# Optimization experiments

Hardware: AMD Instinct MI355X
Metric: run time of the kernel (lower is better)

Reference implementation:

```python
import jax, jax.numpy as jnp
import numpy as np

B, T, I, H, O = 64, 2000, 2, 512, 1
DT, TAU = 10.0, 100.0
EXCIT = 0.8
SIG_REC, SIG_IN = 0.01, 0.01
ALPHA = DT / TAU
IN_SCALE = float(np.sqrt(2.0 * (DT / TAU) * SIG_IN ** 2))
REC_SCALE = float(np.sqrt(2.0 * (TAU / DT) * SIG_REC ** 2))


def setup_inputs() -> dict:
    key = jax.random.key(0)
    ks = jax.random.split(key, 8)
    xav = lambda k, shp, gain: gain * np.sqrt(2.0 / (shp[0] + shp[1])) * jax.random.normal(k, shp, jnp.float32)
    return {
        "i_stim": jax.random.normal(ks[0], (B, T), jnp.float32),
        "i_cc": jax.random.normal(ks[1], (B, T), jnp.float32),
        "hidden": jnp.zeros((B, H), jnp.float32),
        "w_ih": xav(ks[2], (H, I), 1.0),
        "b_ih": jnp.zeros((H,), jnp.float32),
        "w_hh": jax.nn.relu(xav(ks[3], (H, H), 0.1)),  # init applies relu to w_hh
        "b_hh": jnp.zeros((H,), jnp.float32),
        "w_ho": xav(ks[4], (O, H), 1.0),
        "b_ho": jnp.zeros((O,), jnp.float32),
    }


def reference(i_stim, i_cc, hidden, w_ih, b_ih, w_hh, b_hh, w_ho, b_ho):
    ei = jnp.where(jnp.arange(H) < int(EXCIT * H), 1.0, -1.0).astype(w_hh.dtype)
    w_hh_ei = jnp.abs(w_hh * (1.0 - jnp.eye(H, dtype=w_hh.dtype))) * ei  # [H,H], time-invariant

    inputs = jnp.stack([i_stim, i_cc], axis=-1).transpose(1, 0, 2)  # [T,B,2]
    nk = jax.random.key(42)
    n_in = jax.random.normal(jax.random.fold_in(nk, 0), (T, B, I), inputs.dtype)
    n_rec = jax.random.normal(jax.random.fold_in(nk, 1), (T, B, H), hidden.dtype)

    def step(h, xs):
        x_t, ni, nr = xs
        cur = jax.nn.relu(x_t + IN_SCALE * ni)  # training=True path
        hid_in = cur @ w_ih.T  # [B,H]; note b_ih is never added (faithful to source)
        hid_hid = jax.nn.relu(h) @ w_hh_ei.T + b_hh + REC_SCALE * nr
        h_new = h + (-h + hid_in + hid_hid) * ALPHA
        out = jax.nn.relu(h_new) @ w_ho.T + b_ho  # [B,O]
        return h_new, (out, h_new)

    _, (outs, hids) = jax.lax.scan(step, hidden, (inputs, n_in, n_rec))
    return outs.transpose(1, 0, 2), hids.transpose(1, 0, 2)  # [B,T,O], [B,T,H]
```

## Files before the change

kernel.cpp:

```cpp
#include <hip/hip_runtime.h>
#include <stdint.h>
#include <math.h>

#define HH   512
#define BB   64
#define TT   2000
#define NEXC 409
#define SLICE  128
#define NBLK   (BB * 4)

constexpr float ALPHA_F     = 0.1f;
constexpr float IN_SCALE_F  = (float)4.4721359549995794e-03;
constexpr float REC_SCALE_F = (float)4.4721359549995794e-02;
constexpr float SQRT2_F     = 1.41421356237309515f;
constexpr float U_LO        = -0x1.fffffep-1f;

struct U2 { uint32_t a, b; };

__host__ __device__ constexpr uint32_t rotl32(uint32_t x, int d) {
  return (x << d) | (x >> (32 - d));
}

__host__ __device__ constexpr U2 tf2x32(uint32_t k0, uint32_t k1,
                                        uint32_t x0, uint32_t x1) {
  uint32_t ks[3] = {k0, k1, k0 ^ k1 ^ 0x1BD11BDAu};
  const int R[2][4] = {{13, 15, 26, 6}, {17, 29, 16, 24}};
  x0 += ks[0]; x1 += ks[1];
  for (int g = 0; g < 5; ++g) {
    const int* r = R[g & 1];
    for (int i = 0; i < 4; ++i) { x0 += x1; x1 = rotl32(x1, r[i]); x1 ^= x0; }
    x0 += ks[(g + 1) % 3];
    x1 += ks[(g + 2) % 3] + (uint32_t)(g + 1);
  }
  return U2{x0, x1};
}

constexpr U2 KIN_  = tf2x32(0u, 42u, 0u, 0u);
constexpr U2 KREC_ = tf2x32(0u, 42u, 0u, 1u);
constexpr uint32_t KIN0 = KIN_.a,  KIN1 = KIN_.b;
constexpr uint32_t KRC0 = KREC_.a, KRC1 = KREC_.b;

__device__ __forceinline__ float jax_normal(uint32_t k0, uint32_t k1, uint32_t idx) {
  U2 o = tf2x32(k0, k1, 0u, idx);
  uint32_t bits = o.a ^ o.b;
  float f = __uint_as_float((bits >> 9) | 0x3f800000u) - 1.0f;
  float u = fmaxf(U_LO, f * 2.0f + U_LO);
  float w = -log1pf(-u * u);
  float p;
  if (w < 5.0f) {
    w = w - 2.5f;
    p =             2.81022636e-08f;
    p = fmaf(p, w,  3.43273939e-07f);
    p = fmaf(p, w, -3.5233877e-06f);
    p = fmaf(p, w, -4.39150654e-06f);
    p = fmaf(p, w,  0.00021858087f);
    p = fmaf(p, w, -0.00125372503f);
    p = fmaf(p, w, -0.00417768164f);
    p = fmaf(p, w,  0.246640727f);
    p = fmaf(p, w,  1.50140941f);
  } else {
    w = sqrtf(w) - 3.0f;
    p =            -0.000200214257f;
    p = fmaf(p, w,  0.000100950558f);
    p = fmaf(p, w,  0.00134934322f);
    p = fmaf(p, w, -0.00367342844f);
    p = fmaf(p, w,  0.00573950773f);
    p = fmaf(p, w, -0.0076224613f);
    p = fmaf(p, w,  0.00943887047f);
    p = fmaf(p, w,  1.00167406f);
    p = fmaf(p, w,  2.83297682f);
  }
  return SQRT2_F * (p * u);
}

#define PUB_WORDS (2 * BB * HH)
#define PUB_BYTES (PUB_WORDS * 8)

__global__ __launch_bounds__(512, 2)
void zrnn_main(const float* __restrict__ i_stim, const float* __restrict__ i_cc,
               const float* __restrict__ hidden0,
               const float* __restrict__ w_ih, const float* __restrict__ w_hh,
               const float* __restrict__ b_hh,
               const float* __restrict__ w_ho, const float* __restrict__ b_ho,
               float* __restrict__ outs, float* __restrict__ hids,
               uint64_t* __restrict__ pub) {
  const int bid  = blockIdx.x;
  const int low3 = bid & 7;
  const int q    = bid >> 3;
  const int s    = q & 3;
  const int b    = ((q >> 2) << 3) + low3;
  const int tid  = threadIdx.x;
  const int lane = tid & 63;
  const int wv   = tid >> 6;

  const int  ownLo = s * SLICE;
  const bool isOwn = (tid >= ownLo) && (tid < ownLo + SLICE);
  const int  jloc  = tid - ownLo;

  __shared__ float stim_s[TT];
  __shared__ float cc_s[TT];
  __shared__ float red[2][8][SLICE];
  __shared__ float nbuf[4][SLICE];
  __shared__ float nin_s[4][2];
  __shared__ float obuf[8];

  for (int idx = tid; idx < TT; idx += 512) {
    stim_s[idx] = i_stim[b * TT + idx];
    cc_s[idx]   = i_cc[b * TT + idx];
  }

  const int jA = ownLo + lane;
  const int jB = jA + 64;
  const int i0 = wv * 64;
  float wA[64], wB[64];
  #pragma unroll
  for (int k4 = 0; k4 < 16; ++k4) {
    float4 a4 = *reinterpret_cast<const float4*>(&w_hh[jA * HH + i0 + k4 * 4]);
    float4 b4 = *reinterpret_cast<const float4*>(&w_hh[jB * HH + i0 + k4 * 4]);
    const float av[4] = {a4.x, a4.y, a4.z, a4.w};
    const float bv[4] = {b4.x, b4.y, b4.z, b4.w};
    #pragma unroll
    for (int c = 0; c < 4; ++c) {
      const int i = i0 + k4 * 4 + c;
      float va = (i == jA) ? 0.0f : fabsf(av[c]);
      float vb = (i == jB) ? 0.0f : fabsf(bv[c]);
      wA[k4 * 4 + c] = (i < NEXC) ? va : -va;
      wB[k4 * 4 + c] = (i < NEXC) ? vb : -vb;
    }
  }

  float h = 0.0f, wih0 = 0.0f, wih1 = 0.0f, bhh = 0.0f;
  if (isOwn) {
    h    = hidden0[b * HH + tid];
    wih0 = w_ih[tid * 2 + 0];
    wih1 = w_ih[tid * 2 + 1];
    bhh  = b_hh[tid];
  }
  const float who_f = w_ho[tid];
  const float bho   = b_ho[0];

  float rv = fmaxf(hidden0[b * HH + tid], 0.0f);

  if (isOwn) {
    #pragma unroll
    for (int tp = 0; tp < 4; ++tp)
      nbuf[tp][jloc] = jax_normal(KRC0, KRC1,
          (uint32_t)tp * (uint32_t)(BB * HH) + (uint32_t)(b * HH + tid));
    if (jloc < 8)
      nin_s[jloc >> 1][jloc & 1] = jax_normal(KIN0, KIN1,
          (uint32_t)((jloc >> 1) * (BB * 2) + b * 2 + (jloc & 1)));
  }

  uint64_t* pub_b0 = pub + (size_t)b * HH;
  uint64_t* pub_b1 = pub + (size_t)(BB + b) * HH;
  float* __restrict__ hid_out = hids + (size_t)b * TT * HH;

  __syncthreads();

  for (int t = 0; t < TT; ++t) {
    const int par = t & 1;

    if (t > 0 && s == ((t - 1) & 3)) {
      float v = rv * who_f;
      #pragma unroll
      for (int off = 32; off > 0; off >>= 1) v += __shfl_down(v, off);
      if (lane == 0) obuf[wv] = v;
    }

    float nr = 0.0f, ni0 = 0.0f, ni1 = 0.0f, x0 = 0.0f, x1 = 0.0f;
    if (isOwn) {
      nr  = nbuf[t & 3][jloc];
      ni0 = nin_s[t & 3][0];
      ni1 = nin_s[t & 3][1];
      x0  = stim_s[t];
      x1  = cc_s[t];
    }

    float accA = 0.0f, accB = 0.0f;
    #pragma unroll
    for (int k = 0; k < 64; ++k) {
      float rk = __uint_as_float(__builtin_amdgcn_readlane(__float_as_uint(rv), k));
      accA = fmaf(rk, wA[k], accA);
      accB = fmaf(rk, wB[k], accB);
    }
    red[par][wv][lane]      = accA;
    red[par][wv][64 + lane] = accB;
    __syncthreads();

    uint64_t* pub_t = par ? pub_b1 : pub_b0;

    if (isOwn) {
      float acc = red[par][0][jloc];
      #pragma unroll
      for (int w = 1; w < 8; ++w) acc += red[par][w][jloc];
      float hid_hid = acc + bhh + REC_SCALE_F * nr;
      float cur0 = fmaxf(x0 + IN_SCALE_F * ni0, 0.0f);
      float cur1 = fmaxf(x1 + IN_SCALE_F * ni1, 0.0f);
      float hid_in = cur0 * wih0 + cur1 * wih1;
      h = h + (-h + hid_in + hid_hid) * ALPHA_F;
      float r = fmaxf(h, 0.0f);
      uint64_t wd = ((uint64_t)(uint32_t)(t + 1) << 32) |
                    (uint64_t)__float_as_uint(r);
      __hip_atomic_store(&pub_t[tid], wd, __ATOMIC_RELAXED,
                         __HIP_MEMORY_SCOPE_AGENT);
      rv = r;
      __builtin_nontemporal_store(h, hid_out + (size_t)t * HH + tid);

      if (tid == ownLo && t > 0 && s == ((t - 1) & 3)) {
        float psum = ((obuf[0] + obuf[1]) + (obuf[2] + obuf[3])) +
                     ((obuf[4] + obuf[5]) + (obuf[6] + obuf[7]));
        outs[b * TT + (t - 1)] = psum + bho;
      }

      if (t + 4 < TT) {
        nbuf[t & 3][jloc] = jax_normal(KRC0, KRC1,
            (uint32_t)(t + 4) * (uint32_t)(BB * HH) + (uint32_t)(b * HH + tid));
        if (jloc < 2)
          nin_s[t & 3][jloc] = jax_normal(KIN0, KIN1,
              (uint32_t)((t + 4) * (BB * 2) + b * 2 + jloc));
      }
    } else {
      const uint32_t tagw = (uint32_t)(t + 1);
      uint64_t w = __hip_atomic_load(&pub_t[tid], __ATOMIC_RELAXED,
                                     __HIP_MEMORY_SCOPE_AGENT);
      if ((uint32_t)(w >> 32) != tagw) {
        uint64_t w2 = __hip_atomic_load(&pub_t[tid], __ATOMIC_RELAXED,
                                        __HIP_MEMORY_SCOPE_AGENT);
        int spins = 0;
        while ((uint32_t)(w >> 32) != tagw) {
          w = w2;
          if (++spins > 16) __builtin_amdgcn_s_sleep(1);
          w2 = __hip_atomic_load(&pub_t[tid], __ATOMIC_RELAXED,
                                 __HIP_MEMORY_SCOPE_AGENT);
        }
      }
      rv = __uint_as_float((uint32_t)w);
    }
  }

  if (s == ((TT - 1) & 3)) {
    float v = rv * who_f;
    #pragma unroll
    for (int off = 32; off > 0; off >>= 1) v += __shfl_down(v, off);
    if (lane == 0) obuf[wv] = v;
    __syncthreads();
    if (tid == ownLo) {
      float psum = ((obuf[0] + obuf[1]) + (obuf[2] + obuf[3])) +
                   ((obuf[4] + obuf[5]) + (obuf[6] + obuf[7]));
      outs[b * TT + (TT - 1)] = psum + bho;
    }
  }
}

extern "C" void kernel_launch(void* const* d_in, const int* in_sizes, int n_in,
                              void* d_out, int out_size, void* d_ws, size_t ws_size,
                              hipStream_t stream) {
  const float* i_stim = (const float*)d_in[0];
  const float* i_cc   = (const float*)d_in[1];
  const float* hidden = (const float*)d_in[2];
  const float* w_ih   = (const float*)d_in[3];
  const float* w_hh   = (const float*)d_in[5];
  const float* b_hh   = (const float*)d_in[6];
  const float* w_ho   = (const float*)d_in[7];
  const float* b_ho   = (const float*)d_in[8];

  float* outs   = (float*)d_out;
  float* hids   = (float*)d_out + (size_t)BB * TT;
  uint64_t* pub = (uint64_t*)d_ws;

  hipMemsetAsync(pub, 0, PUB_BYTES, stream);

  void* args[] = {(void*)&i_stim, (void*)&i_cc, (void*)&hidden, (void*)&w_ih,
                  (void*)&w_hh, (void*)&b_hh, (void*)&w_ho, (void*)&b_ho,
                  (void*)&outs, (void*)&hids, (void*)&pub};
  hipLaunchCooperativeKernel((const void*)zrnn_main, dim3(NBLK), dim3(512),
                             args, 0, stream);
}
```

Baseline: 4.230 ms.

## Offload noise RNG to idle waves and lighten per-step barrier and spin

Moves generation of the recurrent and input noise off the owner waves, which sit on the critical path. The waiting waves now produce it five steps ahead into an 8-deep LDS ring. The output projection is always reduced by slice-0 blocks using a double-buffered obuf, so the owner epilogue no longer has to write outputs. The __syncthreads is replaced by a barrier that waits only on LDS counters, so it no longer stalls on outstanding global stores. The spin-wait becomes a 4-deep pipelined atomic poll without sleep. Together these aim to shorten the per-timestep serial dependency chain, at the cost of more polling traffic and subtler LDS ordering between waves.

```diff
diff --git a/kernel.cpp b/kernel.cpp
--- a/kernel.cpp
+++ b/kernel.cpp
@@ -73,8 +73,17 @@
   return SQRT2_F * (p * u);
 }
 
-#define PUB_WORDS (2 * BB * HH)
-#define PUB_BYTES (PUB_WORDS * 8)
+#define PUB_BYTES (2 * BB * HH * 8)
+
+__device__ __forceinline__ void barrier_lds() {
+  asm volatile("s_waitcnt lgkmcnt(0)" ::: "memory");
+  __builtin_amdgcn_s_barrier();
+  asm volatile("" ::: "memory");
+}
+
+__device__ __forceinline__ uint64_t pub_ld(const uint64_t* a) {
+  return __hip_atomic_load(a, __ATOMIC_RELAXED, __HIP_MEMORY_SCOPE_AGENT);
+}
 
 __global__ __launch_bounds__(512, 2)
 void zrnn_main(const float* __restrict__ i_stim, const float* __restrict__ i_cc,
@@ -92,17 +101,15 @@
   const int tid  = threadIdx.x;
   const int lane = tid & 63;
   const int wv   = tid >> 6;
-
-  const int  ownLo = s * SLICE;
-  const bool isOwn = (tid >= ownLo) && (tid < ownLo + SLICE);
-  const int  jloc  = tid - ownLo;
+  const int dwv  = (wv - 2 * s) & 7;
+  const int ownLo = s * SLICE;
 
   __shared__ float stim_s[TT];
   __shared__ float cc_s[TT];
   __shared__ float red[2][8][SLICE];
-  __shared__ float nbuf[4][SLICE];
-  __shared__ float nin_s[4][2];
-  __shared__ float obuf[8];
+  __shared__ float nbuf[8][SLICE];
+  __shared__ float nin_s[8][2];
+  __shared__ float obuf[2][8];
 
   for (int idx = tid; idx < TT; idx += 512) {
     stim_s[idx] = i_stim[b * TT + idx];
@@ -130,7 +137,7 @@
   }
 
   float h = 0.0f, wih0 = 0.0f, wih1 = 0.0f, bhh = 0.0f;
-  if (isOwn) {
+  if (dwv < 2) {
     h    = hidden0[b * HH + tid];
     wih0 = w_ih[tid * 2 + 0];
     wih1 = w_ih[tid * 2 + 1];
@@ -141,14 +148,15 @@
 
   float rv = fmaxf(hidden0[b * HH + tid], 0.0f);
 
-  if (isOwn) {
-    #pragma unroll
-    for (int tp = 0; tp < 4; ++tp)
-      nbuf[tp][jloc] = jax_normal(KRC0, KRC1,
-          (uint32_t)tp * (uint32_t)(BB * HH) + (uint32_t)(b * HH + tid));
-    if (jloc < 8)
-      nin_s[jloc >> 1][jloc & 1] = jax_normal(KIN0, KIN1,
-          (uint32_t)((jloc >> 1) * (BB * 2) + b * 2 + (jloc & 1)));
+  for (int e = tid; e < 5 * SLICE; e += 512) {
+    const int tp = e >> 7;
+    const int jn = e & 127;
+    nbuf[tp][jn] = jax_normal(KRC0, KRC1,
+        (uint32_t)tp * (uint32_t)(BB * HH) + (uint32_t)(b * HH + ownLo + jn));
+  }
+  if (tid < 10) {
+    nin_s[tid >> 1][tid & 1] = jax_normal(KIN0, KIN1,
+        (uint32_t)((tid >> 1) * (BB * 2) + b * 2 + (tid & 1)));
   }
 
   uint64_t* pub_b0 = pub + (size_t)b * HH;
@@ -160,20 +168,17 @@
   for (int t = 0; t < TT; ++t) {
     const int par = t & 1;
 
-    if (t > 0 && s == ((t - 1) & 3)) {
+    if (s == 0) {
       float v = rv * who_f;
       #pragma unroll
       for (int off = 32; off > 0; off >>= 1) v += __shfl_down(v, off);
-      if (lane == 0) obuf[wv] = v;
-    }
-
-    float nr = 0.0f, ni0 = 0.0f, ni1 = 0.0f, x0 = 0.0f, x1 = 0.0f;
-    if (isOwn) {
-      nr  = nbuf[t & 3][jloc];
-      ni0 = nin_s[t & 3][0];
-      ni1 = nin_s[t & 3][1];
-      x0  = stim_s[t];
-      x1  = cc_s[t];
+      if (lane == 0) obuf[par][wv] = v;
+      if (dwv == 5 && lane == 0 && t >= 2) {
+        const float* ob = obuf[par ^ 1];
+        float p = ((ob[0] + ob[1]) + (ob[2] + ob[3])) +
+                  ((ob[4] + ob[5]) + (ob[6] + ob[7]));
+        outs[b * TT + (t - 2)] = p + bho;
+      }
     }
 
     float accA = 0.0f, accB = 0.0f;
@@ -185,17 +190,22 @@
     }
     red[par][wv][lane]      = accA;
     red[par][wv][64 + lane] = accB;
-    __syncthreads();
-
-    uint64_t* pub_t = par ? pub_b1 : pub_b0;
-
-    if (isOwn) {
+
+    barrier_lds();
+
+    uint64_t* pub_t = ((t + 1) & 1) ? pub_b1 : pub_b0;
+
+    if (dwv < 2) {
+      const int jloc = tid - ownLo;
       float acc = red[par][0][jloc];
       #pragma unroll
       for (int w = 1; w < 8; ++w) acc += red[par][w][jloc];
+      float nr  = nbuf[t & 7][jloc];
+      float ni0 = nin_s[t & 7][0];
+      float ni1 = nin_s[t & 7][1];
       float hid_hid = acc + bhh + REC_SCALE_F * nr;
-      float cur0 = fmaxf(x0 + IN_SCALE_F * ni0, 0.0f);
-      float cur1 = fmaxf(x1 + IN_SCALE_F * ni1, 0.0f);
+      float cur0 = fmaxf(stim_s[t] + IN_SCALE_F * ni0, 0.0f);
+      float cur1 = fmaxf(cc_s[t]   + IN_SCALE_F * ni1, 0.0f);
       float hid_in = cur0 * wih0 + cur1 * wih1;
       h = h + (-h + hid_in + hid_hid) * ALPHA_F;
       float r = fmaxf(h, 0.0f);
@@ -205,49 +215,52 @@
                          __HIP_MEMORY_SCOPE_AGENT);
       rv = r;
       __builtin_nontemporal_store(h, hid_out + (size_t)t * HH + tid);
-
-      if (tid == ownLo && t > 0 && s == ((t - 1) & 3)) {
-        float psum = ((obuf[0] + obuf[1]) + (obuf[2] + obuf[3])) +
-                     ((obuf[4] + obuf[5]) + (obuf[6] + obuf[7]));
-        outs[b * TT + (t - 1)] = psum + bho;
-      }
-
-      if (t + 4 < TT) {
-        nbuf[t & 3][jloc] = jax_normal(KRC0, KRC1,
-            (uint32_t)(t + 4) * (uint32_t)(BB * HH) + (uint32_t)(b * HH + tid));
-        if (jloc < 2)
-          nin_s[t & 3][jloc] = jax_normal(KIN0, KIN1,
-              (uint32_t)((t + 4) * (BB * 2) + b * 2 + jloc));
-      }
     } else {
-      const uint32_t tagw = (uint32_t)(t + 1);
-      uint64_t w = __hip_atomic_load(&pub_t[tid], __ATOMIC_RELAXED,
-                                     __HIP_MEMORY_SCOPE_AGENT);
-      if ((uint32_t)(w >> 32) != tagw) {
-        uint64_t w2 = __hip_atomic_load(&pub_t[tid], __ATOMIC_RELAXED,
-                                        __HIP_MEMORY_SCOPE_AGENT);
-        int spins = 0;
-        while ((uint32_t)(w >> 32) != tagw) {
-          w = w2;
-          if (++spins > 16) __builtin_amdgcn_s_sleep(1);
-          w2 = __hip_atomic_load(&pub_t[tid], __ATOMIC_RELAXED,
-                                 __HIP_MEMORY_SCOPE_AGENT);
+      if (t + 5 < TT) {
+        if (dwv == 2) {
+          nbuf[(t + 5) & 7][lane] = jax_normal(KRC0, KRC1,
+              (uint32_t)(t + 5) * (uint32_t)(BB * HH) +
+              (uint32_t)(b * HH + ownLo + lane));
+        } else if (dwv == 3) {
+          nbuf[(t + 5) & 7][64 + lane] = jax_normal(KRC0, KRC1,
+              (uint32_t)(t + 5) * (uint32_t)(BB * HH) +
+              (uint32_t)(b * HH + ownLo + 64 + lane));
+        } else if (dwv == 4 && lane < 2) {
+          nin_s[(t + 5) & 7][lane] = jax_normal(KIN0, KIN1,
+              (uint32_t)((t + 5) * (BB * 2) + b * 2 + lane));
         }
       }
-      rv = __uint_as_float((uint32_t)w);
-    }
-  }
-
-  if (s == ((TT - 1) & 3)) {
+      const uint32_t tagw = (uint32_t)(t + 1);
+      const uint64_t* a = &pub_t[tid];
+      uint64_t w0 = pub_ld(a);
+      uint64_t w1 = pub_ld(a);
+      uint64_t w2 = pub_ld(a);
+      uint64_t w3 = pub_ld(a);
+      while ((uint32_t)(w0 >> 32) != tagw) {
+        w0 = w1; w1 = w2; w2 = w3;
+        w3 = pub_ld(a);
+      }
+      rv = __uint_as_float((uint32_t)w0);
+    }
+  }
+
+  if (s == 0) {
+    if (dwv == 5 && lane == 0) {
+      const float* ob = obuf[(TT - 1) & 1];
+      float p = ((ob[0] + ob[1]) + (ob[2] + ob[3])) +
+                ((ob[4] + ob[5]) + (ob[6] + ob[7]));
+      outs[b * TT + (TT - 2)] = p + bho;
+    }
     float v = rv * who_f;
     #pragma unroll
     for (int off = 32; off > 0; off >>= 1) v += __shfl_down(v, off);
-    if (lane == 0) obuf[wv] = v;
+    if (lane == 0) obuf[TT & 1][wv] = v;
     __syncthreads();
-    if (tid == ownLo) {
-      float psum = ((obuf[0] + obuf[1]) + (obuf[2] + obuf[3])) +
-                   ((obuf[4] + obuf[5]) + (obuf[6] + obuf[7]));
-      outs[b * TT + (TT - 1)] = psum + bho;
+    if (dwv == 5 && lane == 0) {
+      const float* ob = obuf[TT & 1];
+      float p = ((ob[0] + ob[1]) + (ob[2] + ob[3])) +
+                ((ob[4] + ob[5]) + (ob[6] + ob[7]));
+      outs[b * TT + (TT - 1)] = p + bho;
     }
   }
 }
```

Measured after the change: 4.587 ms. 1.08x slower.
